# Kernel optimization log

Hardware: AMD Instinct MI355X
Metric: run time of the kernel (lower is better)

Reference implementation:

```python
import jax, jax.numpy as jnp
import numpy as np

EPS = 1e-5
K = 20


def _knn_idx(p, k):
    # p: (B, N, C) -> indices of k nearest neighbors (B, N, k), self included
    inner = jnp.einsum('bnc,bmc->bnm', p, p)
    sq = jnp.sum(p * p, axis=-1)  # (B, N)
    neg_dist = 2.0 * inner - sq[:, :, None] - sq[:, None, :]
    return jax.lax.top_k(neg_dist, k)[1]


def _edge_feature(x, k):
    # x: (B, N, C) -> (B, N, k, 2C) = [neighbor - center, center]
    C = x.shape[-1]
    src = x if C in (3, 6) else x[..., 6:9]  # faithful to torch code path
    idx = _knn_idx(src, k)                    # (B, N, k)
    nb = jax.vmap(lambda xb, ib: xb[ib])(x, idx)  # (B, N, k, C)
    ctr = jnp.broadcast_to(x[:, :, None, :], nb.shape)
    return jnp.concatenate([nb - ctr, ctr], axis=-1)


def _block(h, W, g, b, m, v):
    # 1x1 conv (channels-last) + eval-mode BatchNorm + LeakyReLU(0.2)
    z = jnp.einsum('...c,oc->...o', h, W)
    z = (z - m) * jax.lax.rsqrt(v + EPS) * g + b
    return jnp.where(z >= 0, z, 0.2 * z)


def setup_inputs() -> dict:
    key = jax.random.key(0)
    B, N, D, F = 8, 2048, 3, 1024
    ks = jax.random.split(key, 16)
    s = 0.1
    x = jax.random.normal(ks[0], (B, N, D), dtype=jnp.float32)
    W1 = jax.random.normal(ks[1], (64, 2 * D), dtype=jnp.float32) * s
    W2 = jax.random.normal(ks[2], (64, 64), dtype=jnp.float32) * s
    W3 = jax.random.normal(ks[3], (64, 128), dtype=jnp.float32) * s
    W4 = jax.random.normal(ks[4], (64, 64), dtype=jnp.float32) * s
    W5 = jax.random.normal(ks[5], (64, 128), dtype=jnp.float32) * s
    W6 = jax.random.normal(ks[6], (F, 192), dtype=jnp.float32) * s
    # BN params for bn1..bn5 stacked along axis 0
    bng = 1.0 + 0.1 * jax.random.normal(ks[7], (5, 64), dtype=jnp.float32)
    bnb = 0.1 * jax.random.normal(ks[8], (5, 64), dtype=jnp.float32)
    bnm = 0.1 * jax.random.normal(ks[9], (5, 64), dtype=jnp.float32)
    bnv = 0.5 + jax.random.uniform(ks[10], (5, 64), dtype=jnp.float32)
    bn6g = 1.0 + 0.1 * jax.random.normal(ks[11], (F,), dtype=jnp.float32)
    bn6b = 0.1 * jax.random.normal(ks[12], (F,), dtype=jnp.float32)
    bn6m = 0.1 * jax.random.normal(ks[13], (F,), dtype=jnp.float32)
    bn6v = 0.5 + jax.random.uniform(ks[14], (F,), dtype=jnp.float32)
    return {"x": x, "W1": W1, "W2": W2, "W3": W3, "W4": W4, "W5": W5,
            "W6": W6, "bng": bng, "bnb": bnb, "bnm": bnm, "bnv": bnv,
            "bn6g": bn6g, "bn6b": bn6b, "bn6m": bn6m, "bn6v": bn6v}


def reference(x, W1, W2, W3, W4, W5, W6, bng, bnb, bnm, bnv,
              bn6g, bn6b, bn6m, bn6v):
    # x: (B, N, 3) channels-last throughout
    e = _edge_feature(x, K)                    # (B, N, K, 6)
    h = _block(e, W1, bng[0], bnb[0], bnm[0], bnv[0])
    h = _block(h, W2, bng[1], bnb[1], bnm[1], bnv[1])
    x1 = jnp.max(h, axis=2)                    # (B, N, 64)

    e = _edge_feature(x1, K)                   # knn on channels 6:9
    h = _block(e, W3, bng[2], bnb[2], bnm[2], bnv[2])
    h = _block(h, W4, bng[3], bnb[3], bnm[3], bnv[3])
    x2 = jnp.max(h, axis=2)                    # (B, N, 64)

    e = _edge_feature(x2, K)
    h = _block(e, W5, bng[4], bnb[4], bnm[4], bnv[4])
    x3 = jnp.max(h, axis=2)                    # (B, N, 64)

    x4 = jnp.concatenate([x1, x2, x3], axis=-1)  # (B, N, 192)
    z = _block(x4, W6, bn6g, bn6b, bn6m, bn6v)   # (B, N, F)
    g = jnp.max(z, axis=1)                       # (B, F)
    feat = g[:, None, :]                         # (B, 1, F)
    return feat, jnp.transpose(x4, (0, 2, 1))    # x4 as (B, 192, N)
```

## Files before the change

kernel.cpp:

```cpp
#include <hip/hip_runtime.h>
#include <hip/hip_bf16.h>
#include <math.h>

#define B_ 8
#define N_ 2048
#define KNN 20
#define CH 64

typedef unsigned int u32;
typedef unsigned short ushort16;
typedef __attribute__((ext_vector_type(8))) short s8v;
typedef __attribute__((ext_vector_type(4))) float f4v;

__device__ __forceinline__ float lrelu(float z) { return z >= 0.0f ? z : 0.2f * z; }

__device__ __forceinline__ u32 enc_f32(float f) {
  u32 u = __float_as_uint(f);
  return (u & 0x80000000u) ? ~u : (u | 0x80000000u);
}
__device__ __forceinline__ float dec_f32(u32 u) {
  u32 bits = (u & 0x80000000u) ? (u ^ 0x80000000u) : ~u;
  return __uint_as_float(bits);
}
__device__ __forceinline__ ushort16 f2bf(float f) {
  u32 u = __float_as_uint(f);
  u = (u + 0x7fffu + ((u >> 16) & 1u)) >> 16;
  return (ushort16)u;
}
__device__ __forceinline__ float bf2f(ushort16 h) { return __uint_as_float(((u32)h) << 16); }

__device__ __forceinline__ void split3(const float* __restrict__ p, s8v& a0, s8v& a1, s8v& a2) {
#pragma unroll
  for (int j = 0; j < 8; ++j) {
    float v = p[j];
    ushort16 h0 = f2bf(v);
    float r = v - bf2f(h0);
    u32 ru = __float_as_uint(r);
    a0[j] = (short)h0;
    a1[j] = (short)(ru >> 16);
    float r2 = r - __uint_as_float(ru & 0xFFFF0000u);
    a2[j] = (short)f2bf(r2);
  }
}

#define MFMA6(ACC, A0, A1, A2, B0, B1, B2)                                   \
  ACC = __builtin_amdgcn_mfma_f32_16x16x32_bf16(A0, B0, ACC, 0, 0, 0);       \
  ACC = __builtin_amdgcn_mfma_f32_16x16x32_bf16(A0, B1, ACC, 0, 0, 0);       \
  ACC = __builtin_amdgcn_mfma_f32_16x16x32_bf16(A1, B0, ACC, 0, 0, 0);       \
  ACC = __builtin_amdgcn_mfma_f32_16x16x32_bf16(A0, B2, ACC, 0, 0, 0);       \
  ACC = __builtin_amdgcn_mfma_f32_16x16x32_bf16(A1, B1, ACC, 0, 0, 0);       \
  ACC = __builtin_amdgcn_mfma_f32_16x16x32_bf16(A2, B0, ACC, 0, 0, 0);

__device__ __forceinline__ void wsplit(float v, ushort16& h0, ushort16& h1, ushort16& h2) {
  h0 = f2bf(v);
  float r = v - bf2f(h0);
  h1 = f2bf(r);
  float r2 = r - bf2f(h1);
  h2 = f2bf(r2);
}

__global__ __launch_bounds__(256) void prep_kernel(
    const float* __restrict__ W2, const float* __restrict__ W3, const float* __restrict__ W4,
    const float* __restrict__ W5, const float* __restrict__ W6,
    float4* __restrict__ w2p, float4* __restrict__ w3p, float4* __restrict__ w4p,
    ushort16* __restrict__ wp5h, ushort16* __restrict__ wp5m, ushort16* __restrict__ wp5l,
    ushort16* __restrict__ wp6h, ushort16* __restrict__ wp6m, ushort16* __restrict__ wp6l,
    u32* __restrict__ gkeys) {
  int i = blockIdx.x * 256 + threadIdx.x;
  if (i < 196608) {
    int j = i & 7, l = (i >> 3) & 63, t = i >> 9;
    int kk = t >> 6, nt = t & 63;
    int d = kk * 32 + ((l >> 4) << 3) + j;
    int ch = nt * 16 + (l & 15);
    ushort16 a, b, c;
    wsplit(W6[ch * 192 + d], a, b, c);
    wp6h[i] = a; wp6m[i] = b; wp6l[i] = c;
  }
  if (i < 8192) {
    gkeys[i] = 0u;
    int j = i & 7, l = (i >> 3) & 63, tile = i >> 9;
    int kk = tile >> 2, nt = tile & 3;
    int d = kk * 32 + ((l >> 4) << 3) + j;
    int ch = nt * 16 + (l & 15);
    float v5 = (d < 64) ? W5[ch * 128 + d] : (W5[ch * 128 + d] - W5[ch * 128 + d - 64]);
    ushort16 a, b, c;
    wsplit(v5, a, b, c); wp5h[i] = a; wp5m[i] = b; wp5l[i] = c;
  }
  if (i < 2048) {
    int g = i >> 6, c_ = i & 63;
    w3p[i] = *(const float4*)&W3[c_ * 128 + 4 * g];
  }
  if (i < 1024) {
    int g = i >> 6, c_ = i & 63;
    w2p[i] = *(const float4*)&W2[c_ * 64 + 4 * g];
    w4p[i] = *(const float4*)&W4[c_ * 64 + 4 * g];
  }
}

#define QPB 32
#define SL 8
#define CSL (N_ / SL)
#define CAP 31

__global__ __launch_bounds__(256) void knn_kernel(const float* __restrict__ p, int ld, int off,
                                                  int* __restrict__ idxout) {
  __shared__ __align__(16) char arena[64640];
  float4* pts = (float4*)arena;
  int* buf = (int*)(arena + 32896);
  double* dls = (double*)arena;
  int* ils = (int*)(arena + 40960);

  const int b = blockIdx.y;
  const float* pb = p + (size_t)b * N_ * ld + off;
  for (int j = threadIdx.x; j < N_; j += 256) {
    pts[j + (j >> 8)] = make_float4(pb[(size_t)j * ld + 0], pb[(size_t)j * ld + 1],
                                    pb[(size_t)j * ld + 2], 0.f);
  }
  __syncthreads();

  const int t = threadIdx.x & 7;
  const int qloc = threadIdx.x >> 3;
  const int q = blockIdx.x * QPB + qloc;
  const float4 qp = pts[q + (q >> 8)];
  const int jb = t * CSL;
  const float4* myp = pts + jb + t;

  float d0 = 1e30f, d1 = 1e30f, d2 = 1e30f;
#pragma unroll 4
  for (int i = 0; i < CSL; ++i) {
    float4 c = myp[i];
    float dx = qp.x - c.x, dy = qp.y - c.y, dz = qp.z - c.z;
    float d = fmaf(dz, dz, fmaf(dy, dy, dx * dx));
    float lo = fminf(d, d0); float hi = fmaxf(d, d0); d0 = lo;
    float m1 = fminf(d1, hi); float c1 = fmaxf(d1, hi); d1 = m1;
    d2 = fminf(d2, c1);
  }
  float thr = d2;
#pragma unroll
  for (int s = 1; s < 8; s <<= 1) thr = fmaxf(thr, __shfl_xor(thr, s));
  thr = thr * 1.0001f + 1e-7f;

  int cnt = 0;
  int* mybuf = buf + threadIdx.x * CAP;
#pragma unroll 4
  for (int i = 0; i < CSL; ++i) {
    float4 c = myp[i];
    float dx = qp.x - c.x, dy = qp.y - c.y, dz = qp.z - c.z;
    float d = fmaf(dz, dz, fmaf(dy, dy, dx * dx));
    if (d <= thr) {
      if (cnt < CAP) mybuf[cnt] = jb + i;
      ++cnt;
    }
  }

  double ld_[KNN]; int li_[KNN];
#pragma unroll
  for (int u = 0; u < KNN; ++u) { ld_[u] = 1e300; li_[u] = 0x7fffffff; }

  const bool ovf = cnt > CAP;
  const int m = ovf ? 0 : cnt;
  for (int e = 0; e < m; ++e) {
    int j = mybuf[e];
    float4 c = pts[j + (j >> 8)];
    double dx = (double)qp.x - (double)c.x;
    double dy = (double)qp.y - (double)c.y;
    double dz = (double)qp.z - (double)c.z;
    double d = dx * dx + dy * dy + dz * dz;
    if (d < ld_[KNN - 1]) {
      ld_[KNN - 1] = d; li_[KNN - 1] = j;
#pragma unroll
      for (int u = KNN - 1; u > 0; --u) {
        if (ld_[u] < ld_[u - 1]) {
          double td = ld_[u]; ld_[u] = ld_[u - 1]; ld_[u - 1] = td;
          int ti = li_[u]; li_[u] = li_[u - 1]; li_[u - 1] = ti;
        }
      }
    }
  }
  if (ovf) {
    for (int i = 0; i < CSL; ++i) {
      int j = jb + i;
      float4 c = myp[i];
      double dx = (double)qp.x - (double)c.x;
      double dy = (double)qp.y - (double)c.y;
      double dz = (double)qp.z - (double)c.z;
      double d = dx * dx + dy * dy + dz * dz;
      if (d < ld_[KNN - 1]) {
        ld_[KNN - 1] = d; li_[KNN - 1] = j;
#pragma unroll
        for (int u = KNN - 1; u > 0; --u) {
          if (ld_[u] < ld_[u - 1]) {
            double td = ld_[u]; ld_[u] = ld_[u - 1]; ld_[u - 1] = td;
            int ti = li_[u]; li_[u] = li_[u - 1]; li_[u - 1] = ti;
          }
        }
      }
    }
  }
  __syncthreads();
#pragma unroll
  for (int u = 0; u < KNN; ++u) {
    dls[threadIdx.x * KNN + u] = ld_[u];
    ils[threadIdx.x * KNN + u] = li_[u];
  }
  __syncthreads();

  if (t == 0) {
    int h0 = 0, h1 = 0, h2 = 0, h3 = 0, h4 = 0, h5 = 0, h6 = 0, h7 = 0;
    const int lb = qloc * 8;
    int* outp = idxout + ((size_t)b * N_ + q) * KNN;
    for (int r = 0; r < KNN; ++r) {
      double bd = 1e301; int bi = 0x7fffffff; int bt = 0;
#define CONSIDER(T, H)                                                     \
      { int li2 = (lb + (T)) * KNN + (H);                                  \
        double dv = dls[li2]; int iv = ils[li2];                           \
        if (dv < bd || (dv == bd && iv < bi)) { bd = dv; bi = iv; bt = (T); } }
      CONSIDER(0, h0) CONSIDER(1, h1) CONSIDER(2, h2) CONSIDER(3, h3)
      CONSIDER(4, h4) CONSIDER(5, h5) CONSIDER(6, h6) CONSIDER(7, h7)
#undef CONSIDER
      outp[r] = bi;
      h0 += (bt == 0); h1 += (bt == 1); h2 += (bt == 2); h3 += (bt == 3);
      h4 += (bt == 4); h5 += (bt == 5); h6 += (bt == 6); h7 += (bt == 7);
    }
  }
}

__global__ __launch_bounds__(256) void stage1_kernel(
    const float* __restrict__ x, const int* __restrict__ idx,
    const float* __restrict__ W1, const float4* __restrict__ w2p,
    const float* __restrict__ g0, const float* __restrict__ b0,
    const float* __restrict__ m0, const float* __restrict__ v0,
    const float* __restrict__ g1, const float* __restrict__ b1,
    const float* __restrict__ m1, const float* __restrict__ v1,
    float* __restrict__ x1out) {
  __shared__ float nbs[4][KNN][3];
  __shared__ float ctrs[4][3];
  __shared__ int sidx[4][KNN];
  __shared__ float h1s[4][KNN * CH];
  const int b = blockIdx.y;
  const int n0 = blockIdx.x * 4;
  const int p = threadIdx.x >> 6, c = threadIdx.x & 63;

  for (int i = threadIdx.x; i < 4 * KNN; i += 256)
    sidx[i / KNN][i % KNN] = idx[((size_t)b * N_ + n0 + i / KNN) * KNN + i % KNN];
  __syncthreads();
  for (int i = threadIdx.x; i < 4 * KNN * 3; i += 256) {
    int pp = i / (KNN * 3), r = i % (KNN * 3), k = r / 3, d = r % 3;
    nbs[pp][k][d] = x[((size_t)b * N_ + sidx[pp][k]) * 3 + d];
  }
  if (threadIdx.x < 12) {
    int pp = threadIdx.x / 3, d = threadIdx.x % 3;
    ctrs[pp][d] = x[((size_t)b * N_ + n0 + pp) * 3 + d];
  }
  __syncthreads();

  float sc0, sh0, sc1, sh1;
  {
    double rs = 1.0 / sqrt((double)v0[c] + 1e-5);
    sc0 = (float)((double)g0[c] * rs); sh0 = b0[c] - m0[c] * sc0;
    rs = 1.0 / sqrt((double)v1[c] + 1e-5);
    sc1 = (float)((double)g1[c] * rs); sh1 = b1[c] - m1[c] * sc1;
  }

  const float cx = ctrs[p][0], cy = ctrs[p][1], cz = ctrs[p][2];
  const float wa0 = W1[c * 6 + 0], wa1 = W1[c * 6 + 1], wa2 = W1[c * 6 + 2];
  const float wb0 = W1[c * 6 + 3], wb1 = W1[c * 6 + 4], wb2 = W1[c * 6 + 5];
  const float cbase = cx * wb0 + cy * wb1 + cz * wb2;

  float h1r[KNN];
#pragma unroll
  for (int k = 0; k < KNN; ++k) {
    float a = (nbs[p][k][0] - cx) * wa0 + (nbs[p][k][1] - cy) * wa1 + (nbs[p][k][2] - cz) * wa2 + cbase;
    h1r[k] = lrelu(a * sc0 + sh0);
  }

  float* hp = h1s[p];
#pragma unroll
  for (int k = 0; k < KNN; ++k) hp[k * CH + c] = h1r[k];

  float acc2[KNN];
#pragma unroll
  for (int k = 0; k < KNN; ++k) acc2[k] = 0.f;
  for (int g = 0; g < 16; ++g) {
    const float4 w = w2p[g * 64 + c];
#pragma unroll
    for (int k = 0; k < KNN; ++k) {
      const float4 hv = *(const float4*)&hp[k * CH + g * 4];
      acc2[k] += hv.x * w.x; acc2[k] += hv.y * w.y; acc2[k] += hv.z * w.z; acc2[k] += hv.w * w.w;
    }
  }
  float mx = -INFINITY;
#pragma unroll
  for (int k = 0; k < KNN; ++k) mx = fmaxf(mx, lrelu(acc2[k] * sc1 + sh1));
  x1out[((size_t)b * N_ + n0 + p) * CH + c] = mx;
}

__global__ __launch_bounds__(256) void stage2_kernel(
    const float* __restrict__ xin, const int* __restrict__ idx,
    const float4* __restrict__ w3p, const float4* __restrict__ w4p,
    const float* __restrict__ g0, const float* __restrict__ b0,
    const float* __restrict__ m0, const float* __restrict__ v0,
    const float* __restrict__ g1, const float* __restrict__ b1,
    const float* __restrict__ m1, const float* __restrict__ v1,
    float* __restrict__ xout) {
  __shared__ float nbs[4][KNN][CH];
  __shared__ float ctrs[4][CH];
  __shared__ int sidx[4][KNN];
  const int b = blockIdx.y, n0 = blockIdx.x * 4;
  const int p = threadIdx.x >> 6, c = threadIdx.x & 63;

  for (int i = threadIdx.x; i < 4 * KNN; i += 256)
    sidx[i / KNN][i % KNN] = idx[((size_t)b * N_ + n0 + i / KNN) * KNN + i % KNN];
  __syncthreads();
  for (int i = threadIdx.x; i < 4 * KNN * 16; i += 256) {
    int pp = i / (KNN * 16), r = i % (KNN * 16), k = r >> 4, d4 = (r & 15) * 4;
    const float4 v = *(const float4*)&xin[((size_t)b * N_ + sidx[pp][k]) * CH + d4];
    *(float4*)&nbs[pp][k][d4] = v;
  }
  for (int i = threadIdx.x; i < 4 * 16; i += 256) {
    int pp = i / 16, d4 = (i % 16) * 4;
    *(float4*)&ctrs[pp][d4] = *(const float4*)&xin[((size_t)b * N_ + n0 + pp) * CH + d4];
  }
  __syncthreads();

  float sc0, sh0, sc1, sh1;
  {
    double rs = 1.0 / sqrt((double)v0[c] + 1e-5);
    sc0 = (float)((double)g0[c] * rs); sh0 = b0[c] - m0[c] * sc0;
    rs = 1.0 / sqrt((double)v1[c] + 1e-5);
    sc1 = (float)((double)g1[c] * rs); sh1 = b1[c] - m1[c] * sc1;
  }

  float acc[KNN];
#pragma unroll
  for (int k = 0; k < KNN; ++k) acc[k] = 0.f;
  float base = 0.f;
#pragma unroll 4
  for (int d = 0; d < CH; d += 4) {
    const float4 wa = w3p[(d >> 2) * 64 + c];
    const float4 wq = w3p[(16 + (d >> 2)) * 64 + c];
    float a0 = wa.x, a1 = wa.y, a2 = wa.z, a3 = wa.w;
    float q0 = wq.x, q1 = wq.y, q2 = wq.z, q3 = wq.w;
    const float4 ct = *(const float4*)&ctrs[p][d];
    base += ct.x * (q0 - a0) + ct.y * (q1 - a1) + ct.z * (q2 - a2) + ct.w * (q3 - a3);
#pragma unroll
    for (int k = 0; k < KNN; ++k) {
      const float4 nb = *(const float4*)&nbs[p][k][d];
      acc[k] += nb.x * a0 + nb.y * a1 + nb.z * a2 + nb.w * a3;
    }
  }
  float h1r[KNN];
#pragma unroll
  for (int k = 0; k < KNN; ++k) h1r[k] = lrelu((acc[k] + base) * sc0 + sh0);

  float* hp = &nbs[p][0][0];
#pragma unroll
  for (int k = 0; k < KNN; ++k) hp[k * CH + c] = h1r[k];

  float acc2[KNN];
#pragma unroll
  for (int k = 0; k < KNN; ++k) acc2[k] = 0.f;
  for (int g = 0; g < 16; ++g) {
    const float4 w = w4p[g * 64 + c];
#pragma unroll
    for (int k = 0; k < KNN; ++k) {
      const float4 hv = *(const float4*)&hp[k * CH + g * 4];
      acc2[k] += hv.x * w.x; acc2[k] += hv.y * w.y; acc2[k] += hv.z * w.z; acc2[k] += hv.w * w.w;
    }
  }
  float mx = -INFINITY;
#pragma unroll
  for (int k = 0; k < KNN; ++k) mx = fmaxf(mx, lrelu(acc2[k] * sc1 + sh1));
  xout[((size_t)b * N_ + n0 + p) * CH + c] = mx;
}

__global__ __launch_bounds__(256) void stage3_kernel(
    const float* __restrict__ xf, const int* __restrict__ idx,
    const ushort16* __restrict__ wpAh, const ushort16* __restrict__ wpAm, const ushort16* __restrict__ wpAl,
    const float* __restrict__ g0, const float* __restrict__ b0,
    const float* __restrict__ m0, const float* __restrict__ v0,
    float* __restrict__ xoutf) {
  __shared__ int sidx[160];
  __shared__ u32 h2k[512];
  const int b = blockIdx.y, n0 = blockIdx.x * 8;
  const int tid = threadIdx.x, l = tid & 63, wv = tid >> 6;

  for (int i = tid; i < 160; i += 256) sidx[i] = idx[((size_t)b * N_ + n0 + i / KNN) * KNN + i % KNN];
  for (int i = tid; i < 512; i += 256) h2k[i] = 0u;
  __syncthreads();

  float sc1[4], sh1[4];
#pragma unroll
  for (int nt = 0; nt < 4; ++nt) {
    int ch = nt * 16 + (l & 15);
    double rs = 1.0 / sqrt((double)v0[ch] + 1e-5);
    sc1[nt] = (float)((double)g0[ch] * rs); sh1[nt] = b0[ch] - m0[ch] * sc1[nt];
  }
  const int lg = (l >> 4) << 3;

  for (int mt = wv; mt < 10; mt += 4) {
    const int row = mt * 16 + (l & 15);
    const int nb = sidx[row];
    const int p = row / KNN;
    const float* xnb = xf + ((size_t)b * N_ + nb) * CH;
    const float* xct = xf + ((size_t)b * N_ + n0 + p) * CH;

    f4v acc[4];
#pragma unroll
    for (int nt = 0; nt < 4; ++nt) acc[nt] = (f4v){0.f, 0.f, 0.f, 0.f};
#pragma unroll
    for (int kk = 0; kk < 4; ++kk) {
      const float* src = (kk < 2) ? (xnb + kk * 32 + lg) : (xct + (kk - 2) * 32 + lg);
      s8v a0, a1, a2;
      split3(src, a0, a1, a2);
#pragma unroll
      for (int nt = 0; nt < 4; ++nt) {
        int wo = ((kk * 4 + nt) * 64 + l) << 3;
        s8v bh = *(const s8v*)&wpAh[wo];
        s8v bm = *(const s8v*)&wpAm[wo];
        s8v bl = *(const s8v*)&wpAl[wo];
        MFMA6(acc[nt], a0, a1, a2, bh, bm, bl)
      }
    }
#pragma unroll
    for (int nt = 0; nt < 4; ++nt)
#pragma unroll
      for (int r = 0; r < 4; ++r) {
        float v = lrelu(acc[nt][r] * sc1[nt] + sh1[nt]);
        int row2 = mt * 16 + ((l >> 4) << 2) + r;
        atomicMax(&h2k[(row2 / KNN) * 64 + nt * 16 + (l & 15)], enc_f32(v));
      }
  }
  __syncthreads();
  for (int i = tid; i < 512; i += 256) {
    size_t o = ((size_t)b * N_ + n0 + (i >> 6)) * CH + (i & 63);
    xoutf[o] = dec_f32(h2k[i]);
  }
}

__global__ __launch_bounds__(256) void stage6_kernel(
    const float* __restrict__ x1, const float* __restrict__ x2, const float* __restrict__ x3,
    const ushort16* __restrict__ wp6h, const ushort16* __restrict__ wp6m, const ushort16* __restrict__ wp6l,
    const float* __restrict__ g6, const float* __restrict__ b6,
    const float* __restrict__ m6, const float* __restrict__ v6,
    u32* __restrict__ gkeys) {
  const int b = blockIdx.y, n0 = blockIdx.x * 32;
  const int tid = threadIdx.x, l = tid & 63, wv = tid >> 6;
  const int r16 = l & 15, lg = (l >> 4) << 3;

  f4v acc[2][16];
#pragma unroll
  for (int m = 0; m < 2; ++m)
#pragma unroll
    for (int nt = 0; nt < 16; ++nt) acc[m][nt] = (f4v){0.f, 0.f, 0.f, 0.f};

  const float* srcs[3] = {x1, x2, x3};
#pragma unroll
  for (int kk = 0; kk < 6; ++kk) {
    const float* src = srcs[kk >> 1];
    const int col = ((kk & 1) << 5) + lg;
    s8v a0[2], a1[2], a2[2];
#pragma unroll
    for (int m = 0; m < 2; ++m)
      split3(src + ((size_t)b * N_ + n0 + m * 16 + r16) * CH + col, a0[m], a1[m], a2[m]);
#pragma unroll
    for (int nt = 0; nt < 16; ++nt) {
      int t = kk * 64 + wv * 16 + nt;
      int wo = (t * 64 + l) << 3;
      s8v bh = *(const s8v*)&wp6h[wo];
      s8v bm = *(const s8v*)&wp6m[wo];
      s8v bl = *(const s8v*)&wp6l[wo];
      MFMA6(acc[0][nt], a0[0], a1[0], a2[0], bh, bm, bl)
      MFMA6(acc[1][nt], a0[1], a1[1], a2[1], bh, bm, bl)
    }
  }

#pragma unroll
  for (int nt = 0; nt < 16; ++nt) {
    const int ch = (wv * 16 + nt) * 16 + r16;
    double rs = 1.0 / sqrt((double)v6[ch] + 1e-5);
    const float sc = (float)((double)g6[ch] * rs);
    const float sh = b6[ch] - m6[ch] * sc;
    float mx = -INFINITY;
#pragma unroll
    for (int m = 0; m < 2; ++m)
#pragma unroll
      for (int r = 0; r < 4; ++r) mx = fmaxf(mx, lrelu(acc[m][nt][r] * sc + sh));
    mx = fmaxf(mx, __shfl_xor(mx, 16));
    mx = fmaxf(mx, __shfl_xor(mx, 32));
    if (l < 16) atomicMax(&gkeys[(size_t)b * 1024 + (wv * 16 + nt) * 16 + l], enc_f32(mx));
  }
}

__global__ __launch_bounds__(256) void feat_kernel(const u32* __restrict__ gkeys, float* __restrict__ out) {
  int i = blockIdx.x * 256 + threadIdx.x;
  if (i < 8192) out[i] = dec_f32(gkeys[i]);
}

__global__ __launch_bounds__(256) void xpose_kernel(
    const float* __restrict__ x1, const float* __restrict__ x2, const float* __restrict__ x3,
    float* __restrict__ out) {
  __shared__ float tile[64][65];
  const int b = blockIdx.y;
  const int n0 = blockIdx.x * 64;
  const float* srcs[3] = {x1, x2, x3};
#pragma unroll
  for (int s = 0; s < 3; ++s) {
    const float* src = srcs[s];
    {
      const int row = threadIdx.x >> 2, cb = (threadIdx.x & 3) * 16;
      const float4* rp = (const float4*)&src[((size_t)b * N_ + n0 + row) * CH + cb];
      float4 v0 = rp[0], v1 = rp[1], v2 = rp[2], v3 = rp[3];
      float* tp = &tile[row][cb];
      tp[0] = v0.x; tp[1] = v0.y; tp[2] = v0.z; tp[3] = v0.w;
      tp[4] = v1.x; tp[5] = v1.y; tp[6] = v1.z; tp[7] = v1.w;
      tp[8] = v2.x; tp[9] = v2.y; tp[10] = v2.z; tp[11] = v2.w;
      tp[12] = v3.x; tp[13] = v3.y; tp[14] = v3.z; tp[15] = v3.w;
    }
    __syncthreads();
    {
      const int n = threadIdx.x & 63;
      const int cg = (threadIdx.x >> 6) * 16;
      for (int c = cg; c < cg + 16; ++c)
        out[((size_t)b * 192 + s * 64 + c) * N_ + n0 + n] = tile[n][c];
    }
    __syncthreads();
  }
}

extern "C" void kernel_launch(void* const* d_in, const int* in_sizes, int n_in,
                              void* d_out, int out_size, void* d_ws, size_t ws_size,
                              hipStream_t stream) {
  const float* x   = (const float*)d_in[0];
  const float* W1  = (const float*)d_in[1];
  const float* W2  = (const float*)d_in[2];
  const float* W3  = (const float*)d_in[3];
  const float* W4  = (const float*)d_in[4];
  const float* W5  = (const float*)d_in[5];
  const float* W6  = (const float*)d_in[6];
  const float* bng = (const float*)d_in[7];
  const float* bnb = (const float*)d_in[8];
  const float* bnm = (const float*)d_in[9];
  const float* bnv = (const float*)d_in[10];
  const float* g6  = (const float*)d_in[11];
  const float* b6  = (const float*)d_in[12];
  const float* m6  = (const float*)d_in[13];
  const float* v6  = (const float*)d_in[14];
  float* out = (float*)d_out;

  float* ws = (float*)d_ws;
  float* x1b  = ws;
  float* x2b  = x1b + 1048576;
  float* x3b  = x2b + 1048576;
  u32*   gkeys = (u32*)(x3b + 1048576);
  int*   idxb  = (int*)(gkeys + 8192);
  ushort16* wp5h = (ushort16*)(idxb + 327680);
  ushort16* wp5m = wp5h + 8192;
  ushort16* wp5l = wp5m + 8192;
  ushort16* wp6h = wp5l + 8192;
  ushort16* wp6m = wp6h + 196608;
  ushort16* wp6l = wp6m + 196608;
  float4* w2p = (float4*)(wp6l + 196608);
  float4* w3p = w2p + 1024;
  float4* w4p = w3p + 2048;

  prep_kernel<<<768, 256, 0, stream>>>(W2, W3, W4, W5, W6,
                                       w2p, w3p, w4p,
                                       wp5h, wp5m, wp5l,
                                       wp6h, wp6m, wp6l, gkeys);

  knn_kernel<<<dim3(N_ / QPB, B_), 256, 0, stream>>>(x, 3, 0, idxb);
  stage1_kernel<<<dim3(N_ / 4, B_), 256, 0, stream>>>(
      x, idxb, W1, w2p,
      bng + 0, bnb + 0, bnm + 0, bnv + 0,
      bng + 64, bnb + 64, bnm + 64, bnv + 64, x1b);

  knn_kernel<<<dim3(N_ / QPB, B_), 256, 0, stream>>>(x1b, 64, 6, idxb);
  stage2_kernel<<<dim3(N_ / 4, B_), 256, 0, stream>>>(
      x1b, idxb, w3p, w4p,
      bng + 128, bnb + 128, bnm + 128, bnv + 128,
      bng + 192, bnb + 192, bnm + 192, bnv + 192, x2b);

  knn_kernel<<<dim3(N_ / QPB, B_), 256, 0, stream>>>(x2b, 64, 6, idxb);
  stage3_kernel<<<dim3(N_ / 8, B_), 256, 0, stream>>>(
      x2b, idxb, wp5h, wp5m, wp5l,
      bng + 256, bnb + 256, bnm + 256, bnv + 256, x3b);

  stage6_kernel<<<dim3(N_ / 32, B_), 256, 0, stream>>>(
      x1b, x2b, x3b, wp6h, wp6m, wp6l, g6, b6, m6, v6, gkeys);
  feat_kernel<<<32, 256, 0, stream>>>(gkeys, out);
  xpose_kernel<<<dim3(N_ / 64, B_), 256, 0, stream>>>(x1b, x2b, x3b, out + 8192);
}
```

Measured before the change: 711.8 us.

## Read half of hidden activations via readlane and gather stage2 neighbors directly from global

In the second 1x1 conv of stages 1 and 2, odd channel groups are now fetched from the wavefront's own registers with readlane broadcasts. Even groups still come from shared memory, splitting the traffic between the LDS and the scalar path. Stage 2 also drops the shared-memory staging of neighbor and center rows and reads them straight from global memory using wave-uniform row indices. This removes a sync and cuts LDS use, but relies on cached uniform global loads and the cost of readlane.

```diff
diff --git a/kernel.cpp b/kernel.cpp
--- a/kernel.cpp
+++ b/kernel.cpp
@@ -28,6 +28,10 @@
   return (ushort16)u;
 }
 __device__ __forceinline__ float bf2f(ushort16 h) { return __uint_as_float(((u32)h) << 16); }
+
+__device__ __forceinline__ float rdlane(float v, int lane) {
+  return __int_as_float(__builtin_amdgcn_readlane(__float_as_int(v), lane));
+}
 
 __device__ __forceinline__ void split3(const float* __restrict__ p, s8v& a0, s8v& a1, s8v& a2) {
 #pragma unroll
@@ -281,12 +285,24 @@
   float acc2[KNN];
 #pragma unroll
   for (int k = 0; k < KNN; ++k) acc2[k] = 0.f;
+#pragma unroll 2
   for (int g = 0; g < 16; ++g) {
     const float4 w = w2p[g * 64 + c];
-#pragma unroll
-    for (int k = 0; k < KNN; ++k) {
-      const float4 hv = *(const float4*)&hp[k * CH + g * 4];
-      acc2[k] += hv.x * w.x; acc2[k] += hv.y * w.y; acc2[k] += hv.z * w.z; acc2[k] += hv.w * w.w;
+    if (g & 1) {
+#pragma unroll
+      for (int k = 0; k < KNN; ++k) {
+        float hx = rdlane(h1r[k], g * 4 + 0);
+        float hy = rdlane(h1r[k], g * 4 + 1);
+        float hz = rdlane(h1r[k], g * 4 + 2);
+        float hw = rdlane(h1r[k], g * 4 + 3);
+        acc2[k] += hx * w.x; acc2[k] += hy * w.y; acc2[k] += hz * w.z; acc2[k] += hw * w.w;
+      }
+    } else {
+#pragma unroll
+      for (int k = 0; k < KNN; ++k) {
+        const float4 hv = *(const float4*)&hp[k * CH + g * 4];
+        acc2[k] += hv.x * w.x; acc2[k] += hv.y * w.y; acc2[k] += hv.z * w.z; acc2[k] += hv.w * w.w;
+      }
     }
   }
   float mx = -INFINITY;
@@ -303,25 +319,19 @@
     const float* __restrict__ g1, const float* __restrict__ b1,
     const float* __restrict__ m1, const float* __restrict__ v1,
     float* __restrict__ xout) {
-  __shared__ float nbs[4][KNN][CH];
-  __shared__ float ctrs[4][CH];
   __shared__ int sidx[4][KNN];
+  __shared__ float h1s[4][KNN * CH];
   const int b = blockIdx.y, n0 = blockIdx.x * 4;
   const int p = threadIdx.x >> 6, c = threadIdx.x & 63;
 
   for (int i = threadIdx.x; i < 4 * KNN; i += 256)
     sidx[i / KNN][i % KNN] = idx[((size_t)b * N_ + n0 + i / KNN) * KNN + i % KNN];
   __syncthreads();
-  for (int i = threadIdx.x; i < 4 * KNN * 16; i += 256) {
-    int pp = i / (KNN * 16), r = i % (KNN * 16), k = r >> 4, d4 = (r & 15) * 4;
-    const float4 v = *(const float4*)&xin[((size_t)b * N_ + sidx[pp][k]) * CH + d4];
-    *(float4*)&nbs[pp][k][d4] = v;
-  }
-  for (int i = threadIdx.x; i < 4 * 16; i += 256) {
-    int pp = i / 16, d4 = (i % 16) * 4;
-    *(float4*)&ctrs[pp][d4] = *(const float4*)&xin[((size_t)b * N_ + n0 + pp) * CH + d4];
-  }
-  __syncthreads();
+
+  int nrow[KNN];
+#pragma unroll
+  for (int k = 0; k < KNN; ++k) nrow[k] = __builtin_amdgcn_readfirstlane(sidx[p][k]);
+  const float* xct = xin + ((size_t)b * N_ + n0 + p) * CH;
 
   float sc0, sh0, sc1, sh1;
   {
@@ -335,17 +345,17 @@
 #pragma unroll
   for (int k = 0; k < KNN; ++k) acc[k] = 0.f;
   float base = 0.f;
-#pragma unroll 4
+#pragma unroll 2
   for (int d = 0; d < CH; d += 4) {
     const float4 wa = w3p[(d >> 2) * 64 + c];
     const float4 wq = w3p[(16 + (d >> 2)) * 64 + c];
     float a0 = wa.x, a1 = wa.y, a2 = wa.z, a3 = wa.w;
     float q0 = wq.x, q1 = wq.y, q2 = wq.z, q3 = wq.w;
-    const float4 ct = *(const float4*)&ctrs[p][d];
+    const float4 ct = *(const float4*)&xct[d];
     base += ct.x * (q0 - a0) + ct.y * (q1 - a1) + ct.z * (q2 - a2) + ct.w * (q3 - a3);
 #pragma unroll
     for (int k = 0; k < KNN; ++k) {
-      const float4 nb = *(const float4*)&nbs[p][k][d];
+      const float4 nb = *(const float4*)&xin[((size_t)b * N_ + nrow[k]) * CH + d];
       acc[k] += nb.x * a0 + nb.y * a1 + nb.z * a2 + nb.w * a3;
     }
   }
@@ -353,19 +363,31 @@
 #pragma unroll
   for (int k = 0; k < KNN; ++k) h1r[k] = lrelu((acc[k] + base) * sc0 + sh0);
 
-  float* hp = &nbs[p][0][0];
+  float* hp = h1s[p];
 #pragma unroll
   for (int k = 0; k < KNN; ++k) hp[k * CH + c] = h1r[k];
 
   float acc2[KNN];
 #pragma unroll
   for (int k = 0; k < KNN; ++k) acc2[k] = 0.f;
+#pragma unroll 2
   for (int g = 0; g < 16; ++g) {
     const float4 w = w4p[g * 64 + c];
-#pragma unroll
-    for (int k = 0; k < KNN; ++k) {
-      const float4 hv = *(const float4*)&hp[k * CH + g * 4];
-      acc2[k] += hv.x * w.x; acc2[k] += hv.y * w.y; acc2[k] += hv.z * w.z; acc2[k] += hv.w * w.w;
+    if (g & 1) {
+#pragma unroll
+      for (int k = 0; k < KNN; ++k) {
+        float hx = rdlane(h1r[k], g * 4 + 0);
+        float hy = rdlane(h1r[k], g * 4 + 1);
+        float hz = rdlane(h1r[k], g * 4 + 2);
+        float hw = rdlane(h1r[k], g * 4 + 3);
+        acc2[k] += hx * w.x; acc2[k] += hy * w.y; acc2[k] += hz * w.z; acc2[k] += hw * w.w;
+      }
+    } else {
+#pragma unroll
+      for (int k = 0; k < KNN; ++k) {
+        const float4 hv = *(const float4*)&hp[k * CH + g * 4];
+        acc2[k] += hv.x * w.x; acc2[k] += hv.y * w.y; acc2[k] += hv.z * w.z; acc2[k] += hv.w * w.w;
+      }
     }
   }
   float mx = -INFINITY;
```

Measured after the change: 766.7 us. 7.7% more time.
